# Kernel tuning notes

Hardware: AMD Instinct MI355X
Metric: run time of the kernel (lower is better)

Reference implementation:

```python
import jax, jax.numpy as jnp
import numpy as np

N, D = 768, 64
EPS = 1e-5

def _ln(x, g, b):
    u = x.mean(-1, keepdims=True)
    s = ((x - u) ** 2).mean(-1, keepdims=True)
    return g * (x - u) / jnp.sqrt(s + EPS) + b

def setup_inputs() -> dict:
    key = jax.random.key(0)
    ks = jax.random.split(key, 16)
    inp = {
        'corr_index': jax.random.normal(ks[0], (N, N, 2), dtype=jnp.float32),
        'nei_index': jax.random.randint(ks[1], (N, N), 0, 2, dtype=jnp.int32),
        'nei_num': jax.random.randint(ks[2], (N,), 0, N, dtype=jnp.int32),
        'hidden_state': jax.random.normal(ks[3], (N, D), dtype=jnp.float32),
        'cn': jax.random.normal(ks[4], (N, D), dtype=jnp.float32),
        # relativeLayer: MLP(2 -> D)
        'W_r': jax.random.normal(ks[5], (2, D)) * 0.01, 'b_r': jnp.zeros((D,)),
        'g_r': jnp.ones((D,)), 'be_r': jax.random.normal(ks[6], (D,)) * 0.02,
        # ngate: MLP_gate(3D -> D)
        'W_g': jax.random.normal(ks[7], (3 * D, D)) * 0.01, 'b_g': jnp.zeros((D,)),
        'g_g': jnp.ones((D,)), 'be_g': jax.random.normal(ks[8], (D,)) * 0.02,
        # WAr: MLP(3D -> 1)
        'W_a': jax.random.normal(ks[9], (3 * D, 1)) * 0.01, 'b_a': jnp.zeros((1,)),
        'g_a': jnp.ones((1,)), 'be_a': jnp.abs(jax.random.normal(ks[10], (1,))) * 0.02 + 0.01,
        # weight: MLP(D -> D)
        'W_w': jax.random.normal(ks[11], (D, D)) * 0.01, 'b_w': jnp.zeros((D,)),
        'g_w': jnp.ones((D,)), 'be_w': jax.random.normal(ks[12], (D,)) * 0.02,
    }
    return inp

def reference(corr_index, nei_index, nei_num, hidden_state, cn,
              W_r, b_r, g_r, be_r, W_g, b_g, g_g, be_g,
              W_a, b_a, g_a, be_a, W_w, b_w, g_w, be_w):
    n, d = hidden_state.shape
    mask = nei_index > 0  # [N,N]; (i,j): j is neighbor of i
    # relativeLayer on all pairs (values at masked positions match the torch gather)
    r = jax.nn.relu(_ln(corr_index @ W_r + b_r, g_r, be_r))  # [N,N,D]
    hi = jnp.broadcast_to(hidden_state[:, None, :], (n, n, d))  # hi_t: h[i]
    hj = jnp.broadcast_to(hidden_state[None, :, :], (n, n, d))  # nei_inputs: h[j]
    tmp = jnp.concatenate([r, hi, hj], axis=-1)  # [N,N,3D]
    nGate = jax.nn.sigmoid(_ln(tmp @ W_g + b_g, g_g, be_g))  # [N,N,D]
    tt = jax.nn.relu(_ln(tmp @ W_a + b_a, g_a, be_a))[..., 0]  # [N,N]
    Pos = jnp.where(mask, tt, 0.0)
    Pos = jnp.where(Pos == 0.0, -10000.0, Pos)  # Pos[Pos==0] = -10000
    Pos = jax.nn.softmax(Pos, axis=1)  # masked row-softmax over neighbors j
    # H[i,j] = h[j] * nGate[i,j] * Pos[i,j] at masked pairs, else 0
    H = jnp.where(mask[..., None], hj * nGate * Pos[..., None], 0.0)
    H_sum = jax.nn.relu(_ln(jnp.sum(H, axis=1) @ W_w + b_w, g_w, be_w))  # [N,D]
    C = H_sum + cn
    H_out = hidden_state + jnp.tanh(C)
    return (H_out, C)
```

## Files before the change

kernel.cpp:

```cpp
#include <hip/hip_runtime.h>


#define NN 768
#define DD 64
#define CHP 32
#define NCH 24
#define EPSF 1e-5f

typedef __attribute__((ext_vector_type(8))) short short8;
typedef __attribute__((ext_vector_type(4))) float float4v;
typedef __attribute__((ext_vector_type(2))) float float2v;

__device__ __forceinline__ unsigned short f2bf(float f) {
  unsigned int u = __float_as_uint(f);
  u += 0x7fffu + ((u >> 16) & 1u);
  return (unsigned short)(u >> 16);
}

__global__ __launch_bounds__(256) void prep_kernel(
    const float* __restrict__ hidden, const float* __restrict__ Wg,
    const float* __restrict__ bg, const float* __restrict__ Wr,
    const float* __restrict__ br, const float* __restrict__ gr,
    const float* __restrict__ ber, const float* __restrict__ gg,
    const float* __restrict__ beg, const int* __restrict__ nei,
    float* __restrict__ A_pre, float2v* __restrict__ BH,
    float4v* __restrict__ KT, float2v* __restrict__ GB,
    float* __restrict__ evec, unsigned short* __restrict__ WgT,
    unsigned short* __restrict__ Lst, int* __restrict__ cnt_g) {
  const int bid = blockIdx.x;
  const int tid = threadIdx.x;

  if (bid < NN) {
    __shared__ int cLds;
    if (tid == 0) cLds = 0;
    __syncthreads();
#pragma unroll
    for (int rep = 0; rep < 3; ++rep) {
      int jj = tid + rep * 256;
      if (nei[bid * NN + jj] > 0) {
        int idx = atomicAdd(&cLds, 1);
        Lst[bid * NN + idx] = (unsigned short)jj;
      }
    }
    __syncthreads();
    if (tid == 0) cnt_g[bid] = cLds;
    return;
  }

  if (bid == NN) {
    for (int idx = tid; idx < DD * DD; idx += 256) {
      int n = idx >> 6, k = idx & 63;
      WgT[idx] = f2bf(Wg[k * DD + n]);
    }
    if (tid < 64) {
      int t = tid;
      float w0 = Wr[t], w1 = Wr[DD + t], bb = br[t];
      float m0 = w0, m1 = w1, mb = bb;
      for (int m = 1; m < 64; m <<= 1) {
        m0 += __shfl_xor(m0, m);
        m1 += __shfl_xor(m1, m);
        mb += __shfl_xor(mb, m);
      }
      m0 *= (1.f / DD);
      m1 *= (1.f / DD);
      mb *= (1.f / DD);
      float a0 = w0 - m0, a1 = w1 - m1, ab = bb - mb;
      float grt = gr[t];
      float4v kt;
      kt[0] = grt * a0;
      kt[1] = grt * a1;
      kt[2] = grt * ab;
      kt[3] = ber[t];
      KT[t] = kt;
      float2v gb;
      gb[0] = gg[t];
      gb[1] = beg[t];
      GB[t] = gb;
      float e00 = a0 * a0, e11 = a1 * a1, ebb = ab * ab;
      float e01 = a0 * a1, e0b = a0 * ab, e1b = a1 * ab;
      for (int m = 1; m < 64; m <<= 1) {
        e00 += __shfl_xor(e00, m);
        e11 += __shfl_xor(e11, m);
        ebb += __shfl_xor(ebb, m);
        e01 += __shfl_xor(e01, m);
        e0b += __shfl_xor(e0b, m);
        e1b += __shfl_xor(e1b, m);
      }
      if (t == 0) {
        evec[0] = e00 * (1.f / DD);
        evec[1] = e11 * (1.f / DD);
        evec[2] = ebb * (1.f / DD);
        evec[3] = e01 * (1.f / DD);
        evec[4] = e0b * (1.f / DD);
        evec[5] = e1b * (1.f / DD);
      }
    }
    return;
  }

  const int w = tid >> 6;
  const int lane = tid & 63;
  const int i = (bid - NN - 1) * 4 + w;
  float hv = hidden[i * DD + lane];
  float a = bg[lane];
  float b = 0.f;
#pragma unroll 8
  for (int k = 0; k < DD; ++k) {
    float hk = __shfl(hv, k);
    a = fmaf(hk, Wg[(DD + k) * DD + lane], a);
    b = fmaf(hk, Wg[(2 * DD + k) * DD + lane], b);
  }
  A_pre[i * DD + lane] = a;
  float2v bh2;
  bh2[0] = b;
  bh2[1] = hv;
  BH[i * DD + lane] = bh2;
}

__global__ __launch_bounds__(256) void pair_kernel(
    const float2v* __restrict__ corr2, const float* __restrict__ A_pre,
    const float2v* __restrict__ BH, const float4v* __restrict__ KT,
    const float2v* __restrict__ GB, const float* __restrict__ evec,
    const unsigned short* __restrict__ WgT,
    const unsigned short* __restrict__ Lst, const int* __restrict__ cnt_g,
    float* __restrict__ Hpart) {
  __shared__ __align__(16) unsigned short Rt[4][CHP * 72];

  const int b = blockIdx.x;
  const int tid = threadIdx.x;
  const int wid = tid >> 6;
  const int i = b / 6;
  const int c = (b - i * 6) * 4 + wid;
  const int cnt = cnt_g[i];
  const int base = c * CHP;
  if (base >= cnt) return;

  const int lane = tid & 63;
  const int quad = lane >> 4;
  const int nl = lane & 15;
  const int p32 = lane & 31;
  const int h = lane >> 5;

  int pg = base + p32;
  int jp = (int)Lst[i * NN + (pg < cnt ? pg : base)];
  float2v cc = corr2[i * NN + jp];
  const float e00 = evec[0], e11 = evec[1], ebb = evec[2];
  const float e01 = evec[3], e0b = evec[4], e1b = evec[5];
  float var = cc[0] * cc[0] * e00 + cc[1] * cc[1] * e11 + ebb +
              2.f * (cc[0] * cc[1] * e01 + cc[0] * e0b + cc[1] * e1b);
  float iv = rsqrtf(var + EPSF);

  short8 Bf[2][4];
#pragma unroll
  for (int ks = 0; ks < 2; ++ks)
#pragma unroll
    for (int nt = 0; nt < 4; ++nt)
      __builtin_memcpy(&Bf[ks][nt],
                       &WgT[(nt * 16 + nl) * DD + ks * 32 + quad * 8], 16);

  float gg4[4], beg4[4], pre4[4];
#pragma unroll
  for (int nt = 0; nt < 4; ++nt) {
    int d = nt * 16 + nl;
    float2v gb = GB[d];
    gg4[nt] = gb[0];
    beg4[nt] = gb[1];
    pre4[nt] = A_pre[i * DD + d];
  }

  {
    short8 wbuf;
#pragma unroll
    for (int kk = 0; kk < 32; ++kk) {
      float4v kt = KT[h * 32 + kk];
      float s3 = fmaf(cc[0], kt[0], fmaf(cc[1], kt[1], kt[2]));
      float r = fmaxf(0.f, fmaf(iv, s3, kt[3]));
      wbuf[kk & 7] = (short)f2bf(r);
      if ((kk & 7) == 7)
        __builtin_memcpy(&Rt[wid][p32 * 72 + h * 32 + (kk & ~7)], &wbuf, 16);
    }
  }
  __builtin_amdgcn_fence(__ATOMIC_ACQ_REL, "workgroup");

  float accT[4] = {0.f, 0.f, 0.f, 0.f};

#pragma unroll
  for (int t = 0; t < 2; ++t) {
    short8 a0, a1;
    __builtin_memcpy(&a0, &Rt[wid][(t * 16 + nl) * 72 + quad * 8], 16);
    __builtin_memcpy(&a1, &Rt[wid][(t * 16 + nl) * 72 + 32 + quad * 8], 16);
    float4v acc[4];
#pragma unroll
    for (int nt = 0; nt < 4; ++nt) {
      float4v z = {0.f, 0.f, 0.f, 0.f};
      z = __builtin_amdgcn_mfma_f32_16x16x32_bf16(a0, Bf[0][nt], z, 0, 0, 0);
      z = __builtin_amdgcn_mfma_f32_16x16x32_bf16(a1, Bf[1][nt], z, 0, 0, 0);
      acc[nt] = z;
    }

    int jpr[4];
    float pv[4];
#pragma unroll
    for (int rr = 0; rr < 4; ++rr) {
      int pl = t * 16 + quad * 4 + rr;
      jpr[rr] = __shfl(jp, pl);
      pv[rr] = (base + pl < cnt) ? 1.f : 0.f;
    }
    float2v bh2[4][4];
#pragma unroll
    for (int rr = 0; rr < 4; ++rr)
#pragma unroll
      for (int nt = 0; nt < 4; ++nt)
        bh2[rr][nt] = BH[jpr[rr] * DD + nt * 16 + nl];

    float y[4][4];
#pragma unroll
    for (int nt = 0; nt < 4; ++nt)
#pragma unroll
      for (int rr = 0; rr < 4; ++rr)
        y[nt][rr] = acc[nt][rr] + pre4[nt] + bh2[rr][nt][0];
#pragma unroll
    for (int rr = 0; rr < 4; ++rr) {
      float s = y[0][rr] + y[1][rr] + y[2][rr] + y[3][rr];
      float qq = y[0][rr] * y[0][rr] + y[1][rr] * y[1][rr] +
                 y[2][rr] * y[2][rr] + y[3][rr] * y[3][rr];
#pragma unroll
      for (int m = 1; m < 16; m <<= 1) {
        s += __shfl_xor(s, m);
        qq += __shfl_xor(qq, m);
      }
      float u = s * (1.f / DD);
      float vv = qq * (1.f / DD) - u * u;
      float inv = rsqrtf(vv + EPSF);
#pragma unroll
      for (int nt = 0; nt < 4; ++nt) {
        float g = fmaf(gg4[nt], (y[nt][rr] - u) * inv, beg4[nt]);
        float gate = __frcp_rn(1.f + __expf(-g));
        accT[nt] = fmaf(gate * pv[rr], bh2[rr][nt][1], accT[nt]);
      }
    }
  }

#pragma unroll
  for (int nt = 0; nt < 4; ++nt) {
    accT[nt] += __shfl_xor(accT[nt], 16);
    accT[nt] += __shfl_xor(accT[nt], 32);
  }
  if (lane < 16) {
#pragma unroll
    for (int nt = 0; nt < 4; ++nt)
      Hpart[(i * NCH + c) * DD + nt * 16 + nl] = accT[nt];
  }
}

__global__ __launch_bounds__(64) void final_kernel(
    const float* __restrict__ hidden, const float* __restrict__ cn,
    const float* __restrict__ bea, const float* __restrict__ Ww,
    const float* __restrict__ bw, const float* __restrict__ gw,
    const float* __restrict__ bew, const int* __restrict__ cnt_g,
    const float* __restrict__ Hpart, float* __restrict__ out) {
  const int i = blockIdx.x;
  const int d = threadIdx.x;
  const int cnt = cnt_g[i];
  const int nch = (cnt + CHP - 1) >> 5;
  float hs = 0.f;
  for (int c = 0; c < nch; ++c) hs += Hpart[(i * NCH + c) * DD + d];
  float tta = fmaxf(bea[0], 0.f);
  float wgt = (tta > 0.f && cnt > 0) ? (1.f / (float)cnt) : (1.f / (float)NN);
  hs *= wgt;

  float dotv = bw[d];
#pragma unroll 8
  for (int k = 0; k < DD; ++k) {
    float hk = __shfl(hs, k);
    dotv = fmaf(hk, Ww[k * DD + d], dotv);
  }
  float s = dotv, qq = dotv * dotv;
#pragma unroll
  for (int m = 1; m < 64; m <<= 1) {
    s += __shfl_xor(s, m);
    qq += __shfl_xor(qq, m);
  }
  float u = s * (1.f / DD);
  float var = qq * (1.f / DD) - u * u;
  float inv = rsqrtf(var + EPSF);
  float val = fmaxf(0.f, fmaf(gw[d], (dotv - u) * inv, bew[d]));
  float Cv = val + cn[i * DD + d];
  float Ho = hidden[i * DD + d] + tanhf(Cv);
  out[i * DD + d] = Ho;
  out[NN * DD + i * DD + d] = Cv;
}

extern "C" void kernel_launch(void* const* d_in, const int* in_sizes, int n_in,
                              void* d_out, int out_size, void* d_ws,
                              size_t ws_size, hipStream_t stream) {
  const float* corr = (const float*)d_in[0];
  const int* nei = (const int*)d_in[1];
  const float* hidden = (const float*)d_in[3];
  const float* cn = (const float*)d_in[4];
  const float* Wr = (const float*)d_in[5];
  const float* br = (const float*)d_in[6];
  const float* gr = (const float*)d_in[7];
  const float* ber = (const float*)d_in[8];
  const float* Wg = (const float*)d_in[9];
  const float* bg = (const float*)d_in[10];
  const float* gg = (const float*)d_in[11];
  const float* beg = (const float*)d_in[12];
  const float* bea = (const float*)d_in[16];
  const float* Ww = (const float*)d_in[17];
  const float* bw = (const float*)d_in[18];
  const float* gw = (const float*)d_in[19];
  const float* bew = (const float*)d_in[20];
  float* out = (float*)d_out;

  float* ws = (float*)d_ws;
  float* A_pre = ws;
  float2v* BH = (float2v*)(ws + 49152);
  float4v* KT = (float4v*)(ws + 147456);
  float2v* GB = (float2v*)(ws + 147712);
  float* evec = ws + 147840;
  unsigned short* WgT = (unsigned short*)(ws + 147856);
  int* cnt_g = (int*)(ws + 149904);
  unsigned short* Lst = (unsigned short*)(ws + 150672);
  float* Hpart = ws + 445584;

  prep_kernel<<<NN + 1 + NN / 4, 256, 0, stream>>>(
      hidden, Wg, bg, Wr, br, gr, ber, gg, beg, nei, A_pre, BH, KT, GB, evec,
      WgT, Lst, cnt_g);
  pair_kernel<<<NN * 6, 256, 0, stream>>>((const float2v*)corr, A_pre, BH, KT,
                                          GB, evec, WgT, Lst, cnt_g, Hpart);
  final_kernel<<<NN, 64, 0, stream>>>(hidden, cn, bea, Ww, bw, gw, bew, cnt_g,
                                      Hpart, out);
}
```

Before: 150.3 us.

## Fuse final reduction into pair kernel via last-wave atomic counter

Removes the separate final kernel launch. Each pair wave bumps a per-row atomic counter, and the last active wave for row i sums the partials and runs the output MLP, LayerNorm and tanh. Rows with no neighbours are handled directly in the prep kernel. The change also moves the BH gather loads ahead of the MFMAs to hide their latency, and swaps in hardware exp2, rcp and rsq intrinsics for the sigmoid, tanh and rsqrt. In exchange it adds atomics and agent-scope fences, and the fast math is slightly less accurate.

```diff
diff --git a/kernel.cpp b/kernel.cpp
--- a/kernel.cpp
+++ b/kernel.cpp
@@ -6,6 +6,7 @@
 #define CHP 32
 #define NCH 24
 #define EPSF 1e-5f
+#define LOG2E 1.44269504f
 
 typedef __attribute__((ext_vector_type(8))) short short8;
 typedef __attribute__((ext_vector_type(4))) float float4v;
@@ -15,6 +16,16 @@
   unsigned int u = __float_as_uint(f);
   u += 0x7fffu + ((u >> 16) & 1u);
   return (unsigned short)(u >> 16);
+}
+
+__device__ __forceinline__ float fast_sigmoid(float x) {
+  float e = __builtin_amdgcn_exp2f(-LOG2E * x);
+  return __builtin_amdgcn_rcpf(1.f + e);
+}
+
+__device__ __forceinline__ float fast_tanh(float x) {
+  float e = __builtin_amdgcn_exp2f(fminf(x, 20.f) * (2.f * LOG2E));
+  return (e - 1.f) * __builtin_amdgcn_rcpf(e + 1.f);
 }
 
 __global__ __launch_bounds__(256) void prep_kernel(
@@ -23,10 +34,13 @@
     const float* __restrict__ br, const float* __restrict__ gr,
     const float* __restrict__ ber, const float* __restrict__ gg,
     const float* __restrict__ beg, const int* __restrict__ nei,
+    const float* __restrict__ cn, const float* __restrict__ bw,
+    const float* __restrict__ gw, const float* __restrict__ bew,
     float* __restrict__ A_pre, float2v* __restrict__ BH,
     float4v* __restrict__ KT, float2v* __restrict__ GB,
     float* __restrict__ evec, unsigned short* __restrict__ WgT,
-    unsigned short* __restrict__ Lst, int* __restrict__ cnt_g) {
+    unsigned short* __restrict__ Lst, int* __restrict__ cnt_g,
+    int* __restrict__ done_g, float* __restrict__ out) {
   const int bid = blockIdx.x;
   const int tid = threadIdx.x;
 
@@ -43,7 +57,27 @@
       }
     }
     __syncthreads();
-    if (tid == 0) cnt_g[bid] = cLds;
+    if (tid == 0) {
+      cnt_g[bid] = cLds;
+      done_g[bid] = 0;
+    }
+    if (cLds == 0 && tid < 64) {
+      int d = tid;
+      float dotv = bw[d];
+      float s = dotv, qq = dotv * dotv;
+#pragma unroll
+      for (int m = 1; m < 64; m <<= 1) {
+        s += __shfl_xor(s, m);
+        qq += __shfl_xor(qq, m);
+      }
+      float u = s * (1.f / DD);
+      float var = qq * (1.f / DD) - u * u;
+      float inv = __builtin_amdgcn_rsqf(var + EPSF);
+      float val = fmaxf(0.f, fmaf(gw[d], (dotv - u) * inv, bew[d]));
+      float Cv = val + cn[bid * DD + d];
+      out[bid * DD + d] = hidden[bid * DD + d] + fast_tanh(Cv);
+      out[NN * DD + bid * DD + d] = Cv;
+    }
     return;
   }
 
@@ -123,7 +157,11 @@
     const float2v* __restrict__ GB, const float* __restrict__ evec,
     const unsigned short* __restrict__ WgT,
     const unsigned short* __restrict__ Lst, const int* __restrict__ cnt_g,
-    float* __restrict__ Hpart) {
+    float* __restrict__ Hpart, int* __restrict__ done_g,
+    const float* __restrict__ hidden, const float* __restrict__ cn,
+    const float* __restrict__ bea, const float* __restrict__ Ww,
+    const float* __restrict__ bw, const float* __restrict__ gw,
+    const float* __restrict__ bew, float* __restrict__ out) {
   __shared__ __align__(16) unsigned short Rt[4][CHP * 72];
 
   const int b = blockIdx.x;
@@ -148,7 +186,7 @@
   const float e01 = evec[3], e0b = evec[4], e1b = evec[5];
   float var = cc[0] * cc[0] * e00 + cc[1] * cc[1] * e11 + ebb +
               2.f * (cc[0] * cc[1] * e01 + cc[0] * e0b + cc[1] * e1b);
-  float iv = rsqrtf(var + EPSF);
+  float iv = __builtin_amdgcn_rsqf(var + EPSF);
 
   short8 Bf[2][4];
 #pragma unroll
@@ -186,6 +224,21 @@
 
 #pragma unroll
   for (int t = 0; t < 2; ++t) {
+    int jpr[4];
+    float pv[4];
+#pragma unroll
+    for (int rr = 0; rr < 4; ++rr) {
+      int pl = t * 16 + quad * 4 + rr;
+      jpr[rr] = __shfl(jp, pl);
+      pv[rr] = (base + pl < cnt) ? 1.f : 0.f;
+    }
+    float2v bh2[4][4];
+#pragma unroll
+    for (int rr = 0; rr < 4; ++rr)
+#pragma unroll
+      for (int nt = 0; nt < 4; ++nt)
+        bh2[rr][nt] = BH[jpr[rr] * DD + nt * 16 + nl];
+
     short8 a0, a1;
     __builtin_memcpy(&a0, &Rt[wid][(t * 16 + nl) * 72 + quad * 8], 16);
     __builtin_memcpy(&a1, &Rt[wid][(t * 16 + nl) * 72 + 32 + quad * 8], 16);
@@ -198,21 +251,6 @@
       acc[nt] = z;
     }
 
-    int jpr[4];
-    float pv[4];
-#pragma unroll
-    for (int rr = 0; rr < 4; ++rr) {
-      int pl = t * 16 + quad * 4 + rr;
-      jpr[rr] = __shfl(jp, pl);
-      pv[rr] = (base + pl < cnt) ? 1.f : 0.f;
-    }
-    float2v bh2[4][4];
-#pragma unroll
-    for (int rr = 0; rr < 4; ++rr)
-#pragma unroll
-      for (int nt = 0; nt < 4; ++nt)
-        bh2[rr][nt] = BH[jpr[rr] * DD + nt * 16 + nl];
-
     float y[4][4];
 #pragma unroll
     for (int nt = 0; nt < 4; ++nt)
@@ -231,11 +269,11 @@
       }
       float u = s * (1.f / DD);
       float vv = qq * (1.f / DD) - u * u;
-      float inv = rsqrtf(vv + EPSF);
+      float inv = __builtin_amdgcn_rsqf(vv + EPSF);
 #pragma unroll
       for (int nt = 0; nt < 4; ++nt) {
         float g = fmaf(gg4[nt], (y[nt][rr] - u) * inv, beg4[nt]);
-        float gate = __frcp_rn(1.f + __expf(-g));
+        float gate = fast_sigmoid(g);
         accT[nt] = fmaf(gate * pv[rr], bh2[rr][nt][1], accT[nt]);
       }
     }
@@ -251,22 +289,23 @@
     for (int nt = 0; nt < 4; ++nt)
       Hpart[(i * NCH + c) * DD + nt * 16 + nl] = accT[nt];
   }
-}
-
-__global__ __launch_bounds__(64) void final_kernel(
-    const float* __restrict__ hidden, const float* __restrict__ cn,
-    const float* __restrict__ bea, const float* __restrict__ Ww,
-    const float* __restrict__ bw, const float* __restrict__ gw,
-    const float* __restrict__ bew, const int* __restrict__ cnt_g,
-    const float* __restrict__ Hpart, float* __restrict__ out) {
-  const int i = blockIdx.x;
-  const int d = threadIdx.x;
-  const int cnt = cnt_g[i];
-  const int nch = (cnt + CHP - 1) >> 5;
+
+  __builtin_amdgcn_fence(__ATOMIC_RELEASE, "agent");
+  int old = 0;
+  if (lane == 0)
+    old = __hip_atomic_fetch_add(&done_g[i], 1, __ATOMIC_ACQ_REL,
+                                 __HIP_MEMORY_SCOPE_AGENT);
+  old = __shfl(old, 0);
+  const int nactive = (cnt + CHP - 1) >> 5;
+  if (old != nactive - 1) return;
+  __builtin_amdgcn_fence(__ATOMIC_ACQUIRE, "agent");
+
+  const int d = lane;
   float hs = 0.f;
-  for (int c = 0; c < nch; ++c) hs += Hpart[(i * NCH + c) * DD + d];
+  for (int c2 = 0; c2 < nactive; ++c2) hs += Hpart[(i * NCH + c2) * DD + d];
   float tta = fmaxf(bea[0], 0.f);
-  float wgt = (tta > 0.f && cnt > 0) ? (1.f / (float)cnt) : (1.f / (float)NN);
+  float wgt = (tta > 0.f) ? __builtin_amdgcn_rcpf((float)cnt)
+                          : (1.f / (float)NN);
   hs *= wgt;
 
   float dotv = bw[d];
@@ -282,12 +321,11 @@
     qq += __shfl_xor(qq, m);
   }
   float u = s * (1.f / DD);
-  float var = qq * (1.f / DD) - u * u;
-  float inv = rsqrtf(var + EPSF);
+  float var2 = qq * (1.f / DD) - u * u;
+  float inv = __builtin_amdgcn_rsqf(var2 + EPSF);
   float val = fmaxf(0.f, fmaf(gw[d], (dotv - u) * inv, bew[d]));
   float Cv = val + cn[i * DD + d];
-  float Ho = hidden[i * DD + d] + tanhf(Cv);
-  out[i * DD + d] = Ho;
+  out[i * DD + d] = hidden[i * DD + d] + fast_tanh(Cv);
   out[NN * DD + i * DD + d] = Cv;
 }
 
@@ -323,12 +361,12 @@
   int* cnt_g = (int*)(ws + 149904);
   unsigned short* Lst = (unsigned short*)(ws + 150672);
   float* Hpart = ws + 445584;
+  int* done_g = (int*)(ws + 1625232);
 
   prep_kernel<<<NN + 1 + NN / 4, 256, 0, stream>>>(
-      hidden, Wg, bg, Wr, br, gr, ber, gg, beg, nei, A_pre, BH, KT, GB, evec,
-      WgT, Lst, cnt_g);
-  pair_kernel<<<NN * 6, 256, 0, stream>>>((const float2v*)corr, A_pre, BH, KT,
-                                          GB, evec, WgT, Lst, cnt_g, Hpart);
-  final_kernel<<<NN, 64, 0, stream>>>(hidden, cn, bea, Ww, bw, gw, bew, cnt_g,
-                                      Hpart, out);
-}
+      hidden, Wg, bg, Wr, br, gr, ber, gg, beg, nei, cn, bw, gw, bew, A_pre,
+      BH, KT, GB, evec, WgT, Lst, cnt_g, done_g, out);
+  pair_kernel<<<NN * 6, 256, 0, stream>>>(
+      (const float2v*)corr, A_pre, BH, KT, GB, evec, WgT, Lst, cnt_g, Hpart,
+      done_g, hidden, cn, bea, Ww, bw, gw, bew, out);
+}
```

Result: slower. 506.7 us (+237.1%).
